# Performance work log

Measured on AMD Instinct MI355X. Metric: run time of the kernel, lower is better.

Reference implementation:

```python
import jax, jax.numpy as jnp
import numpy as np

B, N, D, P = 8, 256, 1024, 512  # batch, n_words, input_dim, proj_dim


def setup_inputs() -> dict:
    key = jax.random.key(0)
    ks = jax.random.split(key, 8)
    w = lambda k, shape: (jax.random.normal(k, shape, dtype=jnp.float32) * 0.02)
    return {
        "x": jax.random.normal(ks[0], (B, N, D), dtype=jnp.float32),
        # bigram path
        "Wl": w(ks[1], (P, D)), "bl": jnp.zeros((P,), jnp.float32),
        "Wr": w(ks[2], (P, D)),  # right proj has no bias
        "Wo": w(ks[3], (1, P)), "bo": jnp.zeros((1,), jnp.float32),
        # start builder: Linear -> ReLU -> Linear
        "Ws1": w(ks[4], (P, D)), "bs1": jnp.zeros((P,), jnp.float32),
        "Ws2": w(ks[5], (1, P)), "bs2": jnp.zeros((1,), jnp.float32),
        # end builder
        "We1": w(ks[6], (P, D)), "be1": jnp.zeros((P,), jnp.float32),
        "We2": w(ks[7], (1, P)), "be2": jnp.zeros((1,), jnp.float32),
    }


def reference(x, Wl, bl, Wr, Wo, bo, Ws1, bs1, Ws2, bs2, We1, be1, We2, be2):
    # start / end scorers: [B,N,1]
    start = jax.nn.relu(jnp.einsum('bnd,pd->bnp', x, Ws1) + bs1) @ Ws2.T + bs2
    end = jax.nn.relu(jnp.einsum('bnd,pd->bnp', x, We1) + be1) @ We2.T + be2
    # bigram projections: [B,N,P]
    left = jnp.einsum('bnd,pd->bnp', x, Wl) + bl
    right = jnp.einsum('bnd,pd->bnp', x, Wr)
    # outer-sum: proj[b,i,j,:] = left[b,j,:] + right[b,i,:]  -> [B,N,N,P]
    proj = jax.nn.relu(left[:, None, :, :] + right[:, :, None, :])
    bigram = jnp.einsum('bijp,qp->bijq', proj, Wo) + bo  # [B,N,N,1]
    return (bigram, start, end)
```

## Files before the change

kernel.cpp:

```cpp
#include <hip/hip_runtime.h>
#include <hip/hip_fp16.h>

typedef __attribute__((ext_vector_type(8))) short short8;
typedef __attribute__((ext_vector_type(4))) float f32x4;

constexpr int kB = 8;
constexpr int kN = 256;
constexpr int kD = 1024;
constexpr int kP = 512;
constexpr int kM = kB * kN;

__device__ __forceinline__ __half2 pk_max2(__half2 a, __half2 b) {
    unsigned ua = *reinterpret_cast<unsigned*>(&a);
    unsigned ub = *reinterpret_cast<unsigned*>(&b);
    unsigned ur;
    asm("v_pk_max_f16 %0, %1, %2" : "=v"(ur) : "v"(ua), "v"(ub));
    return *reinterpret_cast<__half2*>(&ur);
}

__global__ __launch_bounds__(256) void cvt_kernel(
    const float* __restrict__ x,
    const float* __restrict__ Wl, const float* __restrict__ Wr,
    const float* __restrict__ Ws1, const float* __restrict__ We1,
    const float* __restrict__ bs2, const float* __restrict__ be2,
    unsigned short* __restrict__ xb, unsigned short* __restrict__ wb,
    float* __restrict__ out_start, float* __restrict__ out_end)
{
    const int bid = blockIdx.x;
    if (bid >= 2048) {
        const int idx = (bid - 2048) * 256 + threadIdx.x;
        if (idx < 2048) out_start[idx] = bs2[0];
        else            out_end[idx - 2048] = be2[0];
        return;
    }
    const int g = bid * 256 + threadIdx.x;
    const float* src;
    unsigned short* dst;
    if (g < 262144) {
        src = x + (size_t)g * 8;
        dst = xb + (size_t)g * 8;
    } else {
        const int gg = g - 262144;
        const int w = gg >> 16;
        const int r = gg & 65535;
        const float* s = (w == 0) ? Wl : (w == 1) ? Wr : (w == 2) ? Ws1 : We1;
        src = s + (size_t)r * 8;
        dst = wb + ((size_t)w << 19) + (size_t)r * 8;
    }
    const float4 a = *reinterpret_cast<const float4*>(src);
    const float4 b = *reinterpret_cast<const float4*>(src + 4);
    const float v[8] = {a.x, a.y, a.z, a.w, b.x, b.y, b.z, b.w};
    short8 o;
#pragma unroll
    for (int i = 0; i < 8; ++i) {
        unsigned u = __float_as_uint(v[i]);
        u = u + 0x7FFF + ((u >> 16) & 1);
        o[i] = (short)(u >> 16);
    }
    *reinterpret_cast<short8*>(dst) = o;
}

__global__ __launch_bounds__(256) void proj_mfma(
    const unsigned short* __restrict__ xb, const unsigned short* __restrict__ wb,
    const float* __restrict__ bl, const float* __restrict__ bs1,
    const float* __restrict__ be1,
    const float* __restrict__ Ws2, const float* __restrict__ We2,
    __half* __restrict__ left_h, __half* __restrict__ right_h,
    float* __restrict__ out_start, float* __restrict__ out_end)
{
    __shared__ unsigned short As[2][128 * 32];
    __shared__ unsigned short Bs[2][64 * 32];

    const int r0 = blockIdx.x * 128;
    const int q0 = blockIdx.y * 64;
    const int z  = q0 >> 9;
    const int t = threadIdx.x, wid = t >> 6, lane = t & 63;
    const int wr = wid >> 1, wc = wid & 1;

    f32x4 acc[4][2] = {};

    const int lrow = lane >> 2, lcol = (lane & 3) * 8;
    const unsigned short* gA0 = xb + (size_t)(r0 + wid * 16 + lrow) * kD + lcol;
    const unsigned short* gA1 = gA0 + (size_t)64 * kD;
    const unsigned short* gB  = wb + (size_t)(q0 + wid * 16 + lrow) * kD + lcol;

#define STAGE(buf, k0) do { \
    __builtin_amdgcn_global_load_lds( \
        (const __attribute__((address_space(1))) void*)(gA0 + (k0)), \
        (__attribute__((address_space(3))) void*)((char*)&As[buf][0] + wid * 1024), 16, 0, 0); \
    __builtin_amdgcn_global_load_lds( \
        (const __attribute__((address_space(1))) void*)(gA1 + (k0)), \
        (__attribute__((address_space(3))) void*)((char*)&As[buf][0] + 4096 + wid * 1024), 16, 0, 0); \
    __builtin_amdgcn_global_load_lds( \
        (const __attribute__((address_space(1))) void*)(gB + (k0)), \
        (__attribute__((address_space(3))) void*)((char*)&Bs[buf][0] + wid * 1024), 16, 0, 0); \
} while (0)

    STAGE(0, 0);
    __syncthreads();
    int cur = 0;
    for (int k0 = 0; k0 < kD; k0 += 32) {
        if (k0 + 32 < kD) STAGE(cur ^ 1, k0 + 32);
        short8 a[4], b[2];
#pragma unroll
        for (int m = 0; m < 4; ++m)
            a[m] = *reinterpret_cast<const short8*>(
                &As[cur][(wr * 64 + m * 16 + (lane & 15)) * 32 + (lane >> 4) * 8]);
#pragma unroll
        for (int n = 0; n < 2; ++n)
            b[n] = *reinterpret_cast<const short8*>(
                &Bs[cur][(wc * 32 + n * 16 + (lane & 15)) * 32 + (lane >> 4) * 8]);
#pragma unroll
        for (int m = 0; m < 4; ++m)
#pragma unroll
            for (int n = 0; n < 2; ++n)
                acc[m][n] = __builtin_amdgcn_mfma_f32_16x16x32_bf16(
                    a[m], b[n], acc[m][n], 0, 0, 0);
        __syncthreads();
        cur ^= 1;
    }
#undef STAGE

    int pcol[2]; float bq[2];
#pragma unroll
    for (int n = 0; n < 2; ++n) {
        pcol[n] = (q0 & 511) + wc * 32 + n * 16 + (lane & 15);
        bq[n] = (z == 0) ? bl[pcol[n]] : (z == 2) ? bs1[pcol[n]]
              : (z == 3) ? be1[pcol[n]] : 0.f;
    }
    if (z < 2) {
        __half* dst = (z == 0) ? left_h : right_h;
        const int bb = r0 >> 8;
        const int jbase = (r0 & 255) + wr * 64 + (lane >> 4) * 4;
#pragma unroll
        for (int n = 0; n < 2; ++n) {
            __half* drow = dst + (size_t)(bb * kP + pcol[n]) * kN;
#pragma unroll
            for (int m = 0; m < 4; ++m) {
                const f32x4 c = acc[m][n];
                __half2 h01 = __floats2half2_rn(c[0] + bq[n], c[1] + bq[n]);
                __half2 h23 = __floats2half2_rn(c[2] + bq[n], c[3] + bq[n]);
                uint2 u;
                u.x = *reinterpret_cast<unsigned*>(&h01);
                u.y = *reinterpret_cast<unsigned*>(&h23);
                *reinterpret_cast<uint2*>(&drow[jbase + m * 16]) = u;
            }
        }
    } else {
        const float* Wv = (z == 2) ? Ws2 : We2;
        float* outh = (z == 2) ? out_start : out_end;
        const float w0 = Wv[pcol[0]], w1 = Wv[pcol[1]];
        const int rbase = r0 + wr * 64 + (lane >> 4) * 4;
#pragma unroll
        for (int m = 0; m < 4; ++m) {
#pragma unroll
            for (int q = 0; q < 4; ++q) {
                float s = fmaxf(acc[m][0][q] + bq[0], 0.f) * w0 +
                          fmaxf(acc[m][1][q] + bq[1], 0.f) * w1;
                s += __shfl_xor(s, 1); s += __shfl_xor(s, 2);
                s += __shfl_xor(s, 4); s += __shfl_xor(s, 8);
                if ((lane & 15) == 0)
                    atomicAdd(&outh[rbase + m * 16 + q], s);
            }
        }
    }
}

__global__ __launch_bounds__(256) void bigram_kernel(
    const __half* __restrict__ left_h, const __half* __restrict__ right_h,
    const float* __restrict__ Wo, float* __restrict__ part)
{
    __shared__ __half ls[64][64];
    __shared__ __half2 rs2[64][64];
    __shared__ __half2 wos[64];

    const int bz = blockIdx.z, b = bz >> 3, pc = bz & 7;
    const int i0 = blockIdx.y * 64, j0 = blockIdx.x * 64;
    const int t = threadIdx.x, wid = t >> 6, lane = t & 63;
    const int tj = t & 15, ti = t >> 4;

    const __half* lbase = left_h  + (size_t)(b * kP + pc * 64) * kN;
    const __half* rbase = right_h + (size_t)(b * kP + pc * 64) * kN;

#pragma unroll
    for (int h = 0; h < 2; ++h) {
        const int row = wid * 16 + h * 8 + (lane >> 3);
        __builtin_amdgcn_global_load_lds(
            (const __attribute__((address_space(1))) void*)
                (lbase + (size_t)row * kN + j0 + (lane & 7) * 8),
            (__attribute__((address_space(3))) void*)
                ((char*)&ls[0][0] + wid * 2048 + h * 1024),
            16, 0, 0);
    }
    uint2 rload[4];
#pragma unroll
    for (int h = 0; h < 4; ++h) {
        const int idx = h * 256 + t, pp = idx >> 4, iq = idx & 15;
        rload[h] = *reinterpret_cast<const uint2*>(&rbase[(size_t)pp * kN + i0 + iq * 4]);
    }
    if (t < 64) wos[t] = __float2half2_rn(Wo[pc * 64 + t]);
#pragma unroll
    for (int h = 0; h < 4; ++h) {
        const int idx = h * 256 + t, pp = idx >> 4, iq = idx & 15;
        const unsigned lo = rload[h].x, hi = rload[h].y;
        uint4 d;
        d.x = (lo & 0xFFFFu) | (lo << 16);
        d.y = (lo >> 16)     | (lo & 0xFFFF0000u);
        d.z = (hi & 0xFFFFu) | (hi << 16);
        d.w = (hi >> 16)     | (hi & 0xFFFF0000u);
        *reinterpret_cast<uint4*>(&rs2[pp][iq * 4]) = d;
    }
    __syncthreads();

    const __half2 zero2 = __float2half2_rn(0.f);
    __half2 acc2[4][2];
#pragma unroll
    for (int ii = 0; ii < 4; ++ii)
#pragma unroll
        for (int jp = 0; jp < 2; ++jp) acc2[ii][jp] = zero2;

#pragma unroll 8
    for (int kk = 0; kk < 64; ++kk) {
        const __half2 wo2 = wos[kk];
        union { uint2 u; __half2 h[2]; } L;
        L.u = *reinterpret_cast<const uint2*>(&ls[kk][tj * 4]);
        union { uint4 u; __half2 h[4]; } R;
        R.u = *reinterpret_cast<const uint4*>(&rs2[kk][ti * 4]);
#pragma unroll
        for (int ii = 0; ii < 4; ++ii)
#pragma unroll
            for (int jp = 0; jp < 2; ++jp) {
                __half2 s = __hadd2(R.h[ii], L.h[jp]);
                s = pk_max2(s, zero2);
                acc2[ii][jp] = __hfma2(s, wo2, acc2[ii][jp]);
            }
    }

    float* po = part + (size_t)bz * 65536;
#pragma unroll
    for (int ii = 0; ii < 4; ++ii) {
        const float2 a = __half22float2(acc2[ii][0]);
        const float2 c = __half22float2(acc2[ii][1]);
        float4 o = {a.x, a.y, c.x, c.y};
        *reinterpret_cast<float4*>(&po[(i0 + ti * 4 + ii) * kN + j0 + tj * 4]) = o;
    }
}

__global__ __launch_bounds__(256) void reduce_kernel(
    const float* __restrict__ part, const float* __restrict__ bo,
    float* __restrict__ out)
{
    const int e4 = blockIdx.x * 256 + threadIdx.x;
    const int e = e4 * 4, b = e >> 16, r = e & 65535;
    const float bias = bo[0];
    float4 acc = {bias, bias, bias, bias};
#pragma unroll
    for (int k = 0; k < 8; ++k) {
        const float4 v = *reinterpret_cast<const float4*>(
            &part[(size_t)(b * 8 + k) * 65536 + r]);
        acc.x += v.x; acc.y += v.y; acc.z += v.z; acc.w += v.w;
    }
    *reinterpret_cast<float4*>(&out[e]) = acc;
}

extern "C" void kernel_launch(void* const* d_in, const int* in_sizes, int n_in,
                              void* d_out, int out_size, void* d_ws, size_t ws_size,
                              hipStream_t stream) {
    const float* x   = (const float*)d_in[0];
    const float* Wl  = (const float*)d_in[1];
    const float* bl  = (const float*)d_in[2];
    const float* Wr  = (const float*)d_in[3];
    const float* Wo  = (const float*)d_in[4];
    const float* bo  = (const float*)d_in[5];
    const float* Ws1 = (const float*)d_in[6];
    const float* bs1 = (const float*)d_in[7];
    const float* Ws2 = (const float*)d_in[8];
    const float* bs2 = (const float*)d_in[9];
    const float* We1 = (const float*)d_in[10];
    const float* be1 = (const float*)d_in[11];
    const float* We2 = (const float*)d_in[12];
    const float* be2 = (const float*)d_in[13];

    float* out        = (float*)d_out;
    float* out_bigram = out;
    float* out_start  = out + (size_t)kB * kN * kN;
    float* out_end    = out_start + (size_t)kB * kN;

    __half* left_h  = (__half*)d_ws;
    __half* right_h = left_h + (size_t)1048576;
    unsigned short* xb = (unsigned short*)((char*)d_ws + (size_t)4 * 1024 * 1024);
    unsigned short* wb = xb + (size_t)2097152;
    float* part = (float*)((char*)d_ws + (size_t)4 * 1024 * 1024);

    cvt_kernel<<<2064, 256, 0, stream>>>(
        x, Wl, Wr, Ws1, We1, bs2, be2, xb, wb, out_start, out_end);

    proj_mfma<<<dim3(16, 32), 256, 0, stream>>>(
        xb, wb, bl, bs1, be1, Ws2, We2, left_h, right_h, out_start, out_end);

    bigram_kernel<<<dim3(4, 4, 64), 256, 0, stream>>>(
        left_h, right_h, Wo, part);

    reduce_kernel<<<512, 256, 0, stream>>>(part, bo, out_bigram);
}
```

Baseline: 138.1 us.

## Retile projection GEMM with swizzled LDS and split bigram P into 32-chunks

The projection GEMM moves from 128x64 tiles with K-step 32 to 64x64 tiles with K-step 64. Its LDS layout now uses an XOR swizzle to cut bank conflicts on the MFMA operand reads, and twice as many blocks are launched to fill the GPU better. The bigram kernel now splits the projection dimension into 16 chunks of 32 instead of 8 of 64, which doubles its block count and halves the work per block. The cost is twice as many partial buffers written to the workspace and read back by the reduce kernel. That roughly doubles the partial-sum memory traffic, and the workspace must be large enough to hold it.

Result: faster. 128.3 us (-7.1%).

```diff
diff --git a/kernel.cpp b/kernel.cpp
--- a/kernel.cpp
+++ b/kernel.cpp
@@ -68,54 +68,69 @@
     __half* __restrict__ left_h, __half* __restrict__ right_h,
     float* __restrict__ out_start, float* __restrict__ out_end)
 {
-    __shared__ unsigned short As[2][128 * 32];
-    __shared__ unsigned short Bs[2][64 * 32];
-
-    const int r0 = blockIdx.x * 128;
+    __shared__ unsigned short As[2][64 * 64];
+    __shared__ unsigned short Bs[2][64 * 64];
+
+    const int r0 = blockIdx.x * 64;
     const int q0 = blockIdx.y * 64;
     const int z  = q0 >> 9;
     const int t = threadIdx.x, wid = t >> 6, lane = t & 63;
     const int wr = wid >> 1, wc = wid & 1;
 
-    f32x4 acc[4][2] = {};
-
-    const int lrow = lane >> 2, lcol = (lane & 3) * 8;
-    const unsigned short* gA0 = xb + (size_t)(r0 + wid * 16 + lrow) * kD + lcol;
-    const unsigned short* gA1 = gA0 + (size_t)64 * kD;
-    const unsigned short* gB  = wb + (size_t)(q0 + wid * 16 + lrow) * kD + lcol;
+    f32x4 acc[2][2] = {};
+
+    const int srow0 = wid * 16 + (lane >> 3);
+    const int scolh = ((lane & 7) ^ (lane >> 3)) << 3;
+    const unsigned short* gA0 = xb + (size_t)(r0 + srow0) * kD + scolh;
+    const unsigned short* gA1 = gA0 + (size_t)8 * kD;
+    const unsigned short* gB0 = wb + (size_t)(q0 + srow0) * kD + scolh;
+    const unsigned short* gB1 = gB0 + (size_t)8 * kD;
 
 #define STAGE(buf, k0) do { \
     __builtin_amdgcn_global_load_lds( \
         (const __attribute__((address_space(1))) void*)(gA0 + (k0)), \
-        (__attribute__((address_space(3))) void*)((char*)&As[buf][0] + wid * 1024), 16, 0, 0); \
+        (__attribute__((address_space(3))) void*)((char*)&As[buf][0] + wid * 2048), 16, 0, 0); \
     __builtin_amdgcn_global_load_lds( \
         (const __attribute__((address_space(1))) void*)(gA1 + (k0)), \
-        (__attribute__((address_space(3))) void*)((char*)&As[buf][0] + 4096 + wid * 1024), 16, 0, 0); \
+        (__attribute__((address_space(3))) void*)((char*)&As[buf][0] + wid * 2048 + 1024), 16, 0, 0); \
     __builtin_amdgcn_global_load_lds( \
-        (const __attribute__((address_space(1))) void*)(gB + (k0)), \
-        (__attribute__((address_space(3))) void*)((char*)&Bs[buf][0] + wid * 1024), 16, 0, 0); \
+        (const __attribute__((address_space(1))) void*)(gB0 + (k0)), \
+        (__attribute__((address_space(3))) void*)((char*)&Bs[buf][0] + wid * 2048), 16, 0, 0); \
+    __builtin_amdgcn_global_load_lds( \
+        (const __attribute__((address_space(1))) void*)(gB1 + (k0)), \
+        (__attribute__((address_space(3))) void*)((char*)&Bs[buf][0] + wid * 2048 + 1024), 16, 0, 0); \
 } while (0)
+
+    const int sw = (lane & 7) << 4;
+    const int cb0 = (lane >> 4) * 16;
+    const int rA = wr * 32 + (lane & 15);
+    const int rB = wc * 32 + (lane & 15);
 
     STAGE(0, 0);
     __syncthreads();
     int cur = 0;
-    for (int k0 = 0; k0 < kD; k0 += 32) {
-        if (k0 + 32 < kD) STAGE(cur ^ 1, k0 + 32);
-        short8 a[4], b[2];
-#pragma unroll
-        for (int m = 0; m < 4; ++m)
-            a[m] = *reinterpret_cast<const short8*>(
-                &As[cur][(wr * 64 + m * 16 + (lane & 15)) * 32 + (lane >> 4) * 8]);
-#pragma unroll
-        for (int n = 0; n < 2; ++n)
-            b[n] = *reinterpret_cast<const short8*>(
-                &Bs[cur][(wc * 32 + n * 16 + (lane & 15)) * 32 + (lane >> 4) * 8]);
-#pragma unroll
-        for (int m = 0; m < 4; ++m)
+    for (int k0 = 0; k0 < kD; k0 += 64) {
+        if (k0 + 64 < kD) STAGE(cur ^ 1, k0 + 64);
+        short8 a[2][2], b[2][2];
+#pragma unroll
+        for (int m = 0; m < 2; ++m)
+#pragma unroll
+            for (int ks = 0; ks < 2; ++ks) {
+                a[m][ks] = *reinterpret_cast<const short8*>(
+                    (const char*)&As[cur][0] +
+                    (rA + m * 16) * 128 + ((ks * 64 + cb0) ^ sw));
+                b[m][ks] = *reinterpret_cast<const short8*>(
+                    (const char*)&Bs[cur][0] +
+                    (rB + m * 16) * 128 + ((ks * 64 + cb0) ^ sw));
+            }
+#pragma unroll
+        for (int m = 0; m < 2; ++m)
 #pragma unroll
             for (int n = 0; n < 2; ++n)
-                acc[m][n] = __builtin_amdgcn_mfma_f32_16x16x32_bf16(
-                    a[m], b[n], acc[m][n], 0, 0, 0);
+#pragma unroll
+                for (int ks = 0; ks < 2; ++ks)
+                    acc[m][n] = __builtin_amdgcn_mfma_f32_16x16x32_bf16(
+                        a[m][ks], b[n][ks], acc[m][n], 0, 0, 0);
         __syncthreads();
         cur ^= 1;
     }
@@ -131,12 +146,12 @@
     if (z < 2) {
         __half* dst = (z == 0) ? left_h : right_h;
         const int bb = r0 >> 8;
-        const int jbase = (r0 & 255) + wr * 64 + (lane >> 4) * 4;
+        const int jbase = (r0 & 255) + wr * 32 + (lane >> 4) * 4;
 #pragma unroll
         for (int n = 0; n < 2; ++n) {
             __half* drow = dst + (size_t)(bb * kP + pcol[n]) * kN;
 #pragma unroll
-            for (int m = 0; m < 4; ++m) {
+            for (int m = 0; m < 2; ++m) {
                 const f32x4 c = acc[m][n];
                 __half2 h01 = __floats2half2_rn(c[0] + bq[n], c[1] + bq[n]);
                 __half2 h23 = __floats2half2_rn(c[2] + bq[n], c[3] + bq[n]);
@@ -150,9 +165,9 @@
         const float* Wv = (z == 2) ? Ws2 : We2;
         float* outh = (z == 2) ? out_start : out_end;
         const float w0 = Wv[pcol[0]], w1 = Wv[pcol[1]];
-        const int rbase = r0 + wr * 64 + (lane >> 4) * 4;
-#pragma unroll
-        for (int m = 0; m < 4; ++m) {
+        const int rbase = r0 + wr * 32 + (lane >> 4) * 4;
+#pragma unroll
+        for (int m = 0; m < 2; ++m) {
 #pragma unroll
             for (int q = 0; q < 4; ++q) {
                 float s = fmaxf(acc[m][0][q] + bq[0], 0.f) * w0 +
@@ -170,37 +185,36 @@
     const __half* __restrict__ left_h, const __half* __restrict__ right_h,
     const float* __restrict__ Wo, float* __restrict__ part)
 {
-    __shared__ __half ls[64][64];
-    __shared__ __half2 rs2[64][64];
-    __shared__ __half2 wos[64];
-
-    const int bz = blockIdx.z, b = bz >> 3, pc = bz & 7;
+    __shared__ __half ls[32][64];
+    __shared__ __half2 rs2[32][64];
+    __shared__ __half2 wos[32];
+
+    const int bz = blockIdx.z, b = bz >> 4, pc = bz & 15;
     const int i0 = blockIdx.y * 64, j0 = blockIdx.x * 64;
     const int t = threadIdx.x, wid = t >> 6, lane = t & 63;
     const int tj = t & 15, ti = t >> 4;
 
-    const __half* lbase = left_h  + (size_t)(b * kP + pc * 64) * kN;
-    const __half* rbase = right_h + (size_t)(b * kP + pc * 64) * kN;
-
-#pragma unroll
-    for (int h = 0; h < 2; ++h) {
-        const int row = wid * 16 + h * 8 + (lane >> 3);
+    const __half* lbase = left_h  + (size_t)(b * kP + pc * 32) * kN;
+    const __half* rbase = right_h + (size_t)(b * kP + pc * 32) * kN;
+
+    {
+        const int row = wid * 8 + (lane >> 3);
         __builtin_amdgcn_global_load_lds(
             (const __attribute__((address_space(1))) void*)
                 (lbase + (size_t)row * kN + j0 + (lane & 7) * 8),
             (__attribute__((address_space(3))) void*)
-                ((char*)&ls[0][0] + wid * 2048 + h * 1024),
+                ((char*)&ls[0][0] + wid * 1024),
             16, 0, 0);
     }
-    uint2 rload[4];
-#pragma unroll
-    for (int h = 0; h < 4; ++h) {
+    uint2 rload[2];
+#pragma unroll
+    for (int h = 0; h < 2; ++h) {
         const int idx = h * 256 + t, pp = idx >> 4, iq = idx & 15;
         rload[h] = *reinterpret_cast<const uint2*>(&rbase[(size_t)pp * kN + i0 + iq * 4]);
     }
-    if (t < 64) wos[t] = __float2half2_rn(Wo[pc * 64 + t]);
-#pragma unroll
-    for (int h = 0; h < 4; ++h) {
+    if (t < 32) wos[t] = __float2half2_rn(Wo[pc * 32 + t]);
+#pragma unroll
+    for (int h = 0; h < 2; ++h) {
         const int idx = h * 256 + t, pp = idx >> 4, iq = idx & 15;
         const unsigned lo = rload[h].x, hi = rload[h].y;
         uint4 d;
@@ -220,7 +234,7 @@
         for (int jp = 0; jp < 2; ++jp) acc2[ii][jp] = zero2;
 
 #pragma unroll 8
-    for (int kk = 0; kk < 64; ++kk) {
+    for (int kk = 0; kk < 32; ++kk) {
         const __half2 wo2 = wos[kk];
         union { uint2 u; __half2 h[2]; } L;
         L.u = *reinterpret_cast<const uint2*>(&ls[kk][tj * 4]);
@@ -255,9 +269,9 @@
     const float bias = bo[0];
     float4 acc = {bias, bias, bias, bias};
 #pragma unroll
-    for (int k = 0; k < 8; ++k) {
+    for (int k = 0; k < 16; ++k) {
         const float4 v = *reinterpret_cast<const float4*>(
-            &part[(size_t)(b * 8 + k) * 65536 + r]);
+            &part[(size_t)(b * 16 + k) * 65536 + r]);
         acc.x += v.x; acc.y += v.y; acc.z += v.z; acc.w += v.w;
     }
     *reinterpret_cast<float4*>(&out[e]) = acc;
@@ -295,10 +309,10 @@
     cvt_kernel<<<2064, 256, 0, stream>>>(
         x, Wl, Wr, Ws1, We1, bs2, be2, xb, wb, out_start, out_end);
 
-    proj_mfma<<<dim3(16, 32), 256, 0, stream>>>(
+    proj_mfma<<<dim3(32, 32), 256, 0, stream>>>(
         xb, wb, bl, bs1, be1, Ws2, We2, left_h, right_h, out_start, out_end);
 
-    bigram_kernel<<<dim3(4, 4, 64), 256, 0, stream>>>(
+    bigram_kernel<<<dim3(4, 4, 128), 256, 0, stream>>>(
         left_h, right_h, Wo, part);
 
     reduce_kernel<<<512, 256, 0, stream>>>(part, bo, out_bigram);
```
